# Optimization experiments

Hardware: AMD Instinct MI355X
Metric: run time of the kernel (lower is better)

## Reference

```python
import jax, jax.numpy as jnp
import numpy as np

IN_C = 128
KEY_C = 128
VAL_C = 128
HEADS = 8
N_CLS = 4

def setup_inputs() -> dict:
    key = jax.random.key(0)
    ks = jax.random.split(key, 10)
    n, c, d, h, w = 2, IN_C, 16, 64, 64
    x = jax.random.normal(ks[0], (n, c, d, h, w), dtype=jnp.float32)
    CLS = jax.random.normal(ks[1], (n, KEY_C, N_CLS), dtype=jnp.float32)
    s = 0.02
    Wk = jax.random.normal(ks[2], (KEY_C, IN_C), dtype=jnp.float32) * s
    bk = jnp.zeros((KEY_C,), dtype=jnp.float32)
    Wq = jax.random.normal(ks[3], (KEY_C, IN_C), dtype=jnp.float32) * s
    bq = jnp.zeros((KEY_C,), dtype=jnp.float32)
    Wv = jax.random.normal(ks[4], (VAL_C, IN_C), dtype=jnp.float32) * s
    bv = jnp.zeros((VAL_C,), dtype=jnp.float32)
    Wr = jax.random.normal(ks[5], (IN_C, VAL_C), dtype=jnp.float32) * s
    br = jnp.zeros((IN_C,), dtype=jnp.float32)
    return {"x": x, "CLS": CLS, "Wk": Wk, "bk": bk, "Wq": Wq, "bq": bq,
            "Wv": Wv, "bv": bv, "Wr": Wr, "br": br}

def reference(x, CLS, Wk, bk, Wq, bq, Wv, bv, Wr, br):
    n, c, d, h, w = x.shape
    L = d * h * w
    xf = x.reshape(n, c, L)
    # 1x1 Conv3d == channel matmul
    keys = jnp.einsum('oc,ncl->nol', Wk, xf) + bk[None, :, None]
    queries = jnp.einsum('oc,ncl->nol', Wq, xf) + bq[None, :, None]
    values = jnp.einsum('oc,ncl->nol', Wv, xf) + bv[None, :, None]
    # prepend CLS tokens along the sequence axis
    keys = jnp.concatenate([CLS, keys], axis=-1)      # (n, kc, L+4)
    queries = jnp.concatenate([CLS, queries], axis=-1)
    values = jnp.concatenate([CLS, values], axis=-1)
    Lt = L + N_CLS
    hk = KEY_C // HEADS
    hv = VAL_C // HEADS
    # contiguous channel slices per head == reshape (n, HEADS, hk, Lt)
    k = jax.nn.softmax(keys.reshape(n, HEADS, hk, Lt), axis=3)    # softmax over sequence
    q = jax.nn.softmax(queries.reshape(n, HEADS, hk, Lt), axis=2) # softmax over head channels
    v = values.reshape(n, HEADS, hv, Lt)
    context = jnp.einsum('nhkl,nhvl->nhkv', k, v)                 # (n, H, hk, hv)
    att = jnp.einsum('nhkv,nhkl->nhvl', context, q)               # (n, H, hv, Lt)
    # original loop reassigns CLS each head; final value comes from last head
    CLS_out = att[:, -1, :, :N_CLS]                               # (n, hv, 4)
    agg = att[:, :, :, N_CLS:].reshape(n, HEADS * hv, L)          # concat over heads
    attention = (jnp.einsum('oc,ncl->nol', Wr, agg) + br[None, :, None]).reshape(n, c, d, h, w)
    context_last = context[:, -1]                                 # last head's context
    return (attention, context_last, CLS_out)
```

## Files before the change

kernel.cpp:

```cpp
#include <hip/hip_runtime.h>

typedef unsigned short u16;
typedef short bf16x8 __attribute__((ext_vector_type(8)));
typedef float floatx4 __attribute__((ext_vector_type(4)));

#define OUT_CTX 16777216
#define OUT_CLS (OUT_CTX + 512)

__device__ __forceinline__ u16 f2b(float f) {
  unsigned int u = __float_as_uint(f);
  u += 0x7fffu + ((u >> 16) & 1u);
  return (u16)(u >> 16);
}
__device__ __forceinline__ float b2f(u16 b) { return __uint_as_float(((unsigned int)b) << 16); }

__device__ __forceinline__ float pack_val(const float* W, int eo) {
  int mt = eo >> 11;
  int rem = eo & 2047;
  int ks = rem >> 9;
  int lane = (rem >> 3) & 63;
  int j = rem & 7;
  int row = mt * 16 + (lane & 15);
  int col = ks * 32 + (lane >> 4) * 8 + j;
  return W[row * 128 + col];
}

__global__ __launch_bounds__(256) void kP(
    const float* __restrict__ Wk, const float* __restrict__ Wq,
    const float* __restrict__ Wv, const float* __restrict__ CLS,
    float* __restrict__ S2, float* __restrict__ Cnum2,
    u16* __restrict__ wkv, u16* __restrict__ wqf) {
  const int t = threadIdx.x;
  if (blockIdx.x < 24) {
    #pragma unroll
    for (int i = 0; i < 8; ++i) {
      int e = blockIdx.x * 2048 + i * 256 + t;
      if (e < 32768) {
        wkv[e] = f2b(pack_val(e < 16384 ? Wk : Wv, e & 16383));
      } else {
        wqf[e - 32768] = f2b(pack_val(Wq, e - 32768));
      }
    }
  } else {
    int nn = t >> 7, r = t & 127;
    float s = 0.f;
    #pragma unroll
    for (int j = 0; j < 4; ++j) s += __expf(CLS[(nn * 128 + r) * 4 + j]);
    S2[t] = s;
    S2[256 + t] = 0.f;
    S2[512 + t] = 0.f;
    S2[768 + t] = 0.f;
    for (int i = 0; i < 16; ++i) {
      int o = t * 16 + i;
      int n2 = o >> 11;
      int rem = o & 2047;
      int h = rem >> 8;
      int kc = (rem >> 4) & 15;
      int vc = rem & 15;
      float a = 0.f;
      #pragma unroll
      for (int j = 0; j < 4; ++j)
        a += __expf(CLS[(n2 * 128 + h * 16 + kc) * 4 + j]) *
             CLS[(n2 * 128 + h * 16 + vc) * 4 + j];
      Cnum2[o] = a;
      Cnum2[4096 + o] = 0.f;
      Cnum2[8192 + o] = 0.f;
      Cnum2[12288 + o] = 0.f;
    }
  }
}

__global__ __launch_bounds__(256) void kA(
    const float* __restrict__ x, const float* __restrict__ bk,
    const float* __restrict__ bv, float* __restrict__ S2,
    float* __restrict__ Cnum2, const u16* __restrict__ wkv) {
  __shared__ __align__(16) u16 xT[2][64][136];
  __shared__ __align__(16) u16 ev[256][72];
  const int t = threadIdx.x;
  const int w = t >> 6, lane = t & 63;
  const int quad = lane >> 4, lm = lane & 15;
  const int n = blockIdx.x >> 9;
  const int l0base = (blockIdx.x & 511) << 7;
  const int slot = blockIdx.x & 3;
  const int sc = t >> 4;
  const int sl4 = t & 15;

  float4 pf[8];
  #pragma unroll
  for (int i = 0; i < 8; ++i) {
    int c = i * 16 + sc;
    pf[i] = *(const float4*)(x + (((size_t)(n * 128 + c)) << 16) + l0base + sl4 * 4);
  }

  bf16x8 wf[4][4];
  #pragma unroll
  for (int mt = 0; mt < 4; ++mt) {
    int rb = (mt < 2) ? (2 * w + mt) : (8 + 2 * w + (mt - 2));
    #pragma unroll
    for (int ks = 0; ks < 4; ++ks)
      wf[mt][ks] = *(const bf16x8*)(wkv + (((rb * 4 + ks) * 64 + lane) * 8));
  }
  float bias_[4][4];
  #pragma unroll
  for (int mt = 0; mt < 4; ++mt)
    #pragma unroll
    for (int j = 0; j < 4; ++j) {
      int r = w * 32 + (mt & 1) * 16 + quad * 4 + j;
      bias_[mt][j] = (mt < 2) ? bk[r] : bv[r];
    }

  floatx4 z4 = {0.f, 0.f, 0.f, 0.f};
  floatx4 cacc[2] = {z4, z4};
  float sacc[2][4] = {{0.f, 0.f, 0.f, 0.f}, {0.f, 0.f, 0.f, 0.f}};

  for (int tile = 0; tile < 2; ++tile) {
    u16 (*xb)[136] = xT[tile];
    #pragma unroll
    for (int i = 0; i < 8; ++i) {
      int cc = i * 16 + sc;
      int col = sl4 * 4;
      xb[col + 0][cc] = f2b(pf[i].x);
      xb[col + 1][cc] = f2b(pf[i].y);
      xb[col + 2][cc] = f2b(pf[i].z);
      xb[col + 3][cc] = f2b(pf[i].w);
    }
    __syncthreads();

    floatx4 acc[4][4];
    #pragma unroll
    for (int mt = 0; mt < 4; ++mt)
      #pragma unroll
      for (int nt = 0; nt < 4; ++nt) acc[mt][nt] = z4;

    #pragma unroll
    for (int nt = 0; nt < 4; ++nt)
      #pragma unroll
      for (int ks = 0; ks < 4; ++ks) {
        bf16x8 b = *(const bf16x8*)(&xb[nt * 16 + lm][ks * 32 + quad * 8]);
        #pragma unroll
        for (int mt = 0; mt < 4; ++mt)
          acc[mt][nt] = __builtin_amdgcn_mfma_f32_16x16x32_bf16(wf[mt][ks], b, acc[mt][nt], 0, 0, 0);
      }

    if (tile == 0) {
      #pragma unroll
      for (int i = 0; i < 8; ++i) {
        int c = i * 16 + sc;
        pf[i] = *(const float4*)(x + (((size_t)(n * 128 + c)) << 16) + l0base + 64 + sl4 * 4);
      }
    }

    #pragma unroll
    for (int mt = 0; mt < 4; ++mt)
      #pragma unroll
      for (int j = 0; j < 4; ++j) {
        int R = ((mt < 2) ? 0 : 128) + w * 32 + (mt & 1) * 16 + quad * 4 + j;
        #pragma unroll
        for (int nt = 0; nt < 4; ++nt) {
          float v = acc[mt][nt][j] + bias_[mt][j];
          if (mt < 2) {
            v = __expf(v);
            u16 b = f2b(v);
            ev[R][nt * 16 + lm] = b;
            sacc[mt][j] += b2f(b);
          } else {
            ev[R][nt * 16 + lm] = f2b(v);
          }
        }
      }

    #pragma unroll
    for (int hh = 0; hh < 2; ++hh) {
      int h = w * 2 + hh;
      #pragma unroll
      for (int ks = 0; ks < 2; ++ks) {
        bf16x8 aE = *(const bf16x8*)(&ev[h * 16 + lm][ks * 32 + quad * 8]);
        bf16x8 bV = *(const bf16x8*)(&ev[128 + h * 16 + lm][ks * 32 + quad * 8]);
        cacc[hh] = __builtin_amdgcn_mfma_f32_16x16x32_bf16(aE, bV, cacc[hh], 0, 0, 0);
      }
    }
  }

  float* Cn = Cnum2 + slot * 4096;
  #pragma unroll
  for (int hh = 0; hh < 2; ++hh) {
    int h = w * 2 + hh;
    #pragma unroll
    for (int j = 0; j < 4; ++j)
      atomicAdd(&Cn[((n * 8 + h) * 16 + quad * 4 + j) * 16 + lm], cacc[hh][j]);
  }
  #pragma unroll
  for (int mt = 0; mt < 2; ++mt)
    #pragma unroll
    for (int j = 0; j < 4; ++j) {
      float s = sacc[mt][j];
      s += __shfl_xor(s, 1);
      s += __shfl_xor(s, 2);
      s += __shfl_xor(s, 4);
      s += __shfl_xor(s, 8);
      if (lm == 0)
        atomicAdd(&S2[slot * 256 + n * 128 + w * 32 + mt * 16 + quad * 4 + j], s);
    }
}

__global__ __launch_bounds__(256) void kM(
    const float* __restrict__ Wr, const float* __restrict__ CLS,
    const float* __restrict__ S2, const float* __restrict__ Cnum2,
    u16* __restrict__ mfrag, float* __restrict__ out) {
  __shared__ float ctxn[4096];
  const int t = threadIdx.x;
  float sinv = 1.f / (S2[t] + S2[256 + t] + S2[512 + t] + S2[768 + t]);
  #pragma unroll
  for (int i = 0; i < 16; ++i) {
    int o = t * 16 + i;
    ctxn[o] = (Cnum2[o] + Cnum2[4096 + o] + Cnum2[8192 + o] + Cnum2[12288 + o]) * sinv;
  }
  __syncthreads();

  if (blockIdx.x == 0) {
    for (int e = t; e < 512; e += 256) {
      int nn = e >> 8, kc = (e >> 4) & 15, vc = e & 15;
      out[OUT_CTX + e] = ctxn[((nn * 8 + 7) * 16 + kc) * 16 + vc];
    }
    if (t < 128) {
      int nn = t >> 6, vc = (t >> 2) & 15, j = t & 3;
      float den = 0.f, num = 0.f;
      #pragma unroll
      for (int kc = 0; kc < 16; ++kc) {
        float e_ = __expf(CLS[(nn * 128 + 112 + kc) * 4 + j]);
        den += e_;
        num += e_ * ctxn[((nn * 8 + 7) * 16 + kc) * 16 + vc];
      }
      out[OUT_CLS + t] = num / den;
    }
  }

  #pragma unroll
  for (int i = 0; i < 8; ++i) {
    int e = blockIdx.x * 2048 + i * 256 + t;
    int nn = e >> 14;
    int rem = e & 16383;
    int rb = rem >> 11;
    int ks = (rem >> 9) & 3;
    int ln = (rem >> 3) & 63;
    int j = rem & 7;
    int o = rb * 16 + (ln & 15);
    int cc = ks * 32 + (ln >> 4) * 8 + j;
    int h = cc >> 4, k = cc & 15;
    float m = 0.f;
    #pragma unroll
    for (int v = 0; v < 16; ++v)
      m += Wr[o * 128 + h * 16 + v] * ctxn[((nn * 8 + h) * 16 + k) * 16 + v];
    mfrag[e] = f2b(m);
  }
}

__global__ __launch_bounds__(256) void kB(
    const float* __restrict__ x, const float* __restrict__ bq,
    const float* __restrict__ br, const u16* __restrict__ wqf,
    const u16* __restrict__ mfrag, float* __restrict__ out) {
  __shared__ __align__(16) u16 xT[64][136];
  __shared__ __align__(16) u16 qT[64][136];
  const int t = threadIdx.x;
  const int w = t >> 6, lane = t & 63;
  const int quad = lane >> 4, lm = lane & 15;
  const int n = blockIdx.x >> 9;
  const int l0base = (blockIdx.x & 511) << 7;
  const int sc = t >> 4;
  const int sl4 = t & 15;

  float4 pf[8];
  #pragma unroll
  for (int i = 0; i < 8; ++i) {
    int c = i * 16 + sc;
    pf[i] = *(const float4*)(x + (((size_t)(n * 128 + c)) << 16) + l0base + sl4 * 4);
  }

  bf16x8 wq[2][4], mA[2][4];
  #pragma unroll
  for (int mt = 0; mt < 2; ++mt)
    #pragma unroll
    for (int ks = 0; ks < 4; ++ks) {
      wq[mt][ks] = *(const bf16x8*)(wqf + ((((w * 2 + mt) * 4 + ks) * 64 + lane) * 8));
      mA[mt][ks] = *(const bf16x8*)(mfrag + ((((n * 8 + w * 2 + mt) * 4 + ks) * 64 + lane) * 8));
    }

  float bqv_[2][4], brv[2][4];
  #pragma unroll
  for (int mt = 0; mt < 2; ++mt)
    #pragma unroll
    for (int j = 0; j < 4; ++j) {
      bqv_[mt][j] = bq[(w * 2 + mt) * 16 + quad * 4 + j];
      brv[mt][j] = br[(w * 2 + mt) * 16 + quad * 4 + j];
    }

  floatx4 z4 = {0.f, 0.f, 0.f, 0.f};

  for (int tile = 0; tile < 2; ++tile) {
    int l0 = l0base + tile * 64;
    #pragma unroll
    for (int i = 0; i < 8; ++i) {
      int cc = i * 16 + sc;
      int col = sl4 * 4;
      xT[col + 0][cc] = f2b(pf[i].x);
      xT[col + 1][cc] = f2b(pf[i].y);
      xT[col + 2][cc] = f2b(pf[i].z);
      xT[col + 3][cc] = f2b(pf[i].w);
    }
    __syncthreads();

    floatx4 acc[2][4];
    #pragma unroll
    for (int mt = 0; mt < 2; ++mt)
      #pragma unroll
      for (int nt = 0; nt < 4; ++nt) acc[mt][nt] = z4;

    #pragma unroll
    for (int nt = 0; nt < 4; ++nt)
      #pragma unroll
      for (int ks = 0; ks < 4; ++ks) {
        bf16x8 b = *(const bf16x8*)(&xT[nt * 16 + lm][ks * 32 + quad * 8]);
        #pragma unroll
        for (int mt = 0; mt < 2; ++mt)
          acc[mt][nt] = __builtin_amdgcn_mfma_f32_16x16x32_bf16(wq[mt][ks], b, acc[mt][nt], 0, 0, 0);
      }

    #pragma unroll
    for (int mt = 0; mt < 2; ++mt) {
      int h = w * 2 + mt;
      #pragma unroll
      for (int nt = 0; nt < 4; ++nt) {
        float e[4];
        float ssum = 0.f;
        #pragma unroll
        for (int j = 0; j < 4; ++j) {
          e[j] = __expf(acc[mt][nt][j] + bqv_[mt][j]);
          ssum += e[j];
        }
        ssum += __shfl_xor(ssum, 16);
        ssum += __shfl_xor(ssum, 32);
        float inv = 1.f / ssum;
        #pragma unroll
        for (int j = 0; j < 4; ++j)
          qT[nt * 16 + lm][h * 16 + quad * 4 + j] = f2b(e[j] * inv);
      }
    }

    if (tile == 0) {
      #pragma unroll
      for (int i = 0; i < 8; ++i) {
        int c = i * 16 + sc;
        pf[i] = *(const float4*)(x + (((size_t)(n * 128 + c)) << 16) + l0base + 64 + sl4 * 4);
      }
    }
    __syncthreads();

    floatx4 acc2[2][4];
    #pragma unroll
    for (int mt = 0; mt < 2; ++mt)
      #pragma unroll
      for (int nt = 0; nt < 4; ++nt) acc2[mt][nt] = z4;

    #pragma unroll
    for (int nt = 0; nt < 4; ++nt)
      #pragma unroll
      for (int ks = 0; ks < 4; ++ks) {
        bf16x8 b = *(const bf16x8*)(&qT[nt * 16 + lm][ks * 32 + quad * 8]);
        #pragma unroll
        for (int mt = 0; mt < 2; ++mt)
          acc2[mt][nt] = __builtin_amdgcn_mfma_f32_16x16x32_bf16(mA[mt][ks], b, acc2[mt][nt], 0, 0, 0);
      }

    #pragma unroll
    for (int mt = 0; mt < 2; ++mt)
      #pragma unroll
      for (int j = 0; j < 4; ++j) {
        int R = (w * 2 + mt) * 16 + quad * 4 + j;
        #pragma unroll
        for (int nt = 0; nt < 4; ++nt)
          out[(((size_t)(n * 128 + R)) << 16) + l0 + nt * 16 + lm] = acc2[mt][nt][j] + brv[mt][j];
      }
  }
}

extern "C" void kernel_launch(void* const* d_in, const int* in_sizes, int n_in,
                              void* d_out, int out_size, void* d_ws, size_t ws_size,
                              hipStream_t stream) {
  const float* x   = (const float*)d_in[0];
  const float* CLS = (const float*)d_in[1];
  const float* Wk  = (const float*)d_in[2];
  const float* bk  = (const float*)d_in[3];
  const float* Wq  = (const float*)d_in[4];
  const float* bq  = (const float*)d_in[5];
  const float* Wv  = (const float*)d_in[6];
  const float* bv  = (const float*)d_in[7];
  const float* Wr  = (const float*)d_in[8];
  const float* br  = (const float*)d_in[9];
  float* out = (float*)d_out;
  char* ws = (char*)d_ws;
  float* S2    = (float*)(ws + 0);
  float* Cnum2 = (float*)(ws + 4096);
  u16* wkv     = (u16*)(ws + 69632);
  u16* wqf     = (u16*)(ws + 135168);
  u16* mfrag   = (u16*)(ws + 167936);

  kP<<<25, 256, 0, stream>>>(Wk, Wq, Wv, CLS, S2, Cnum2, wkv, wqf);
  kA<<<1024, 256, 0, stream>>>(x, bk, bv, S2, Cnum2, wkv);
  kM<<<16, 256, 0, stream>>>(Wr, CLS, S2, Cnum2, mfrag, out);
  kB<<<1024, 256, 0, stream>>>(x, bq, br, wqf, mfrag, out);
}
```

Before: 195.8 us.

## Drop prep and merge kernels, pack weights inline, recompute context per block

```diff
diff --git a/kernel.cpp b/kernel.cpp
--- a/kernel.cpp
+++ b/kernel.cpp
@@ -2,6 +2,7 @@
 
 typedef unsigned short u16;
 typedef short bf16x8 __attribute__((ext_vector_type(8)));
+typedef short short4v __attribute__((ext_vector_type(4)));
 typedef float floatx4 __attribute__((ext_vector_type(4)));
 
 #define OUT_CTX 16777216
@@ -14,115 +15,70 @@
 }
 __device__ __forceinline__ float b2f(u16 b) { return __uint_as_float(((unsigned int)b) << 16); }
 
-__device__ __forceinline__ float pack_val(const float* W, int eo) {
-  int mt = eo >> 11;
-  int rem = eo & 2047;
-  int ks = rem >> 9;
-  int lane = (rem >> 3) & 63;
-  int j = rem & 7;
-  int row = mt * 16 + (lane & 15);
-  int col = ks * 32 + (lane >> 4) * 8 + j;
-  return W[row * 128 + col];
-}
-
-__global__ __launch_bounds__(256) void kP(
-    const float* __restrict__ Wk, const float* __restrict__ Wq,
-    const float* __restrict__ Wv, const float* __restrict__ CLS,
-    float* __restrict__ S2, float* __restrict__ Cnum2,
-    u16* __restrict__ wkv, u16* __restrict__ wqf) {
-  const int t = threadIdx.x;
-  if (blockIdx.x < 24) {
-    #pragma unroll
-    for (int i = 0; i < 8; ++i) {
-      int e = blockIdx.x * 2048 + i * 256 + t;
-      if (e < 32768) {
-        wkv[e] = f2b(pack_val(e < 16384 ? Wk : Wv, e & 16383));
-      } else {
-        wqf[e - 32768] = f2b(pack_val(Wq, e - 32768));
-      }
-    }
-  } else {
-    int nn = t >> 7, r = t & 127;
-    float s = 0.f;
-    #pragma unroll
-    for (int j = 0; j < 4; ++j) s += __expf(CLS[(nn * 128 + r) * 4 + j]);
-    S2[t] = s;
-    S2[256 + t] = 0.f;
-    S2[512 + t] = 0.f;
-    S2[768 + t] = 0.f;
-    for (int i = 0; i < 16; ++i) {
-      int o = t * 16 + i;
-      int n2 = o >> 11;
-      int rem = o & 2047;
-      int h = rem >> 8;
-      int kc = (rem >> 4) & 15;
-      int vc = rem & 15;
-      float a = 0.f;
-      #pragma unroll
-      for (int j = 0; j < 4; ++j)
-        a += __expf(CLS[(n2 * 128 + h * 16 + kc) * 4 + j]) *
-             CLS[(n2 * 128 + h * 16 + vc) * 4 + j];
-      Cnum2[o] = a;
-      Cnum2[4096 + o] = 0.f;
-      Cnum2[8192 + o] = 0.f;
-      Cnum2[12288 + o] = 0.f;
-    }
-  }
+__device__ __forceinline__ bf16x8 pack8(const float* p) {
+  float4 a = *(const float4*)p;
+  float4 b = *(const float4*)(p + 4);
+  bf16x8 r;
+  r[0] = (short)f2b(a.x); r[1] = (short)f2b(a.y); r[2] = (short)f2b(a.z); r[3] = (short)f2b(a.w);
+  r[4] = (short)f2b(b.x); r[5] = (short)f2b(b.y); r[6] = (short)f2b(b.z); r[7] = (short)f2b(b.w);
+  return r;
+}
+
+__device__ __forceinline__ float dot4(float4 a, float4 b) {
+  return a.x * b.x + a.y * b.y + a.z * b.z + a.w * b.w;
 }
 
 __global__ __launch_bounds__(256) void kA(
-    const float* __restrict__ x, const float* __restrict__ bk,
+    const float* __restrict__ x, const float* __restrict__ Wk,
+    const float* __restrict__ bk, const float* __restrict__ Wv,
     const float* __restrict__ bv, float* __restrict__ S2,
-    float* __restrict__ Cnum2, const u16* __restrict__ wkv) {
-  __shared__ __align__(16) u16 xT[2][64][136];
+    float* __restrict__ Cnum2) {
+  __shared__ __align__(16) u16 xT[64][136];
   __shared__ __align__(16) u16 ev[256][72];
   const int t = threadIdx.x;
   const int w = t >> 6, lane = t & 63;
   const int quad = lane >> 4, lm = lane & 15;
-  const int n = blockIdx.x >> 9;
-  const int l0base = (blockIdx.x & 511) << 7;
-  const int slot = blockIdx.x & 3;
-  const int sc = t >> 4;
-  const int sl4 = t & 15;
+  const int bid = blockIdx.x;
+  const int n = bid >> 8;
+  const int l0base = (bid & 255) << 8;
+  const int slot = bid & 3;
+  const int sc = t >> 4, sl4 = t & 15;
 
   float4 pf[8];
   #pragma unroll
-  for (int i = 0; i < 8; ++i) {
-    int c = i * 16 + sc;
-    pf[i] = *(const float4*)(x + (((size_t)(n * 128 + c)) << 16) + l0base + sl4 * 4);
-  }
+  for (int i = 0; i < 8; ++i)
+    pf[i] = *(const float4*)(x + (((size_t)(n * 128 + sc * 8 + i)) << 16) + l0base + sl4 * 4);
 
   bf16x8 wf[4][4];
   #pragma unroll
-  for (int mt = 0; mt < 4; ++mt) {
-    int rb = (mt < 2) ? (2 * w + mt) : (8 + 2 * w + (mt - 2));
+  for (int nt = 0; nt < 4; ++nt) {
+    const float* W = (nt < 2) ? Wk : Wv;
+    int row = w * 32 + (nt & 1) * 16 + lm;
     #pragma unroll
     for (int ks = 0; ks < 4; ++ks)
-      wf[mt][ks] = *(const bf16x8*)(wkv + (((rb * 4 + ks) * 64 + lane) * 8));
-  }
-  float bias_[4][4];
-  #pragma unroll
-  for (int mt = 0; mt < 4; ++mt)
-    #pragma unroll
-    for (int j = 0; j < 4; ++j) {
-      int r = w * 32 + (mt & 1) * 16 + quad * 4 + j;
-      bias_[mt][j] = (mt < 2) ? bk[r] : bv[r];
-    }
+      wf[nt][ks] = pack8(W + row * 128 + ks * 32 + quad * 8);
+  }
+  float biasE[2] = { bk[w * 32 + lm], bk[w * 32 + 16 + lm] };
+  float biasV[2] = { bv[w * 32 + lm], bv[w * 32 + 16 + lm] };
 
   floatx4 z4 = {0.f, 0.f, 0.f, 0.f};
   floatx4 cacc[2] = {z4, z4};
-  float sacc[2][4] = {{0.f, 0.f, 0.f, 0.f}, {0.f, 0.f, 0.f, 0.f}};
-
-  for (int tile = 0; tile < 2; ++tile) {
-    u16 (*xb)[136] = xT[tile];
-    #pragma unroll
-    for (int i = 0; i < 8; ++i) {
-      int cc = i * 16 + sc;
-      int col = sl4 * 4;
-      xb[col + 0][cc] = f2b(pf[i].x);
-      xb[col + 1][cc] = f2b(pf[i].y);
-      xb[col + 2][cc] = f2b(pf[i].z);
-      xb[col + 3][cc] = f2b(pf[i].w);
+  float sacc[2] = {0.f, 0.f};
+
+  for (int tile = 0; tile < 4; ++tile) {
+    const float* pff = (const float*)pf;
+    #pragma unroll
+    for (int r = 0; r < 4; ++r) {
+      bf16x8 vx;
+      #pragma unroll
+      for (int i = 0; i < 8; ++i) vx[i] = (short)f2b(pff[i * 4 + r]);
+      *(bf16x8*)&xT[sl4 * 4 + r][sc * 8] = vx;
+    }
+    if (tile < 3) {
+      int l0n = l0base + (tile + 1) * 64;
+      #pragma unroll
+      for (int i = 0; i < 8; ++i)
+        pf[i] = *(const float4*)(x + (((size_t)(n * 128 + sc * 8 + i)) << 16) + l0n + sl4 * 4);
     }
     __syncthreads();
 
@@ -133,40 +89,39 @@
       for (int nt = 0; nt < 4; ++nt) acc[mt][nt] = z4;
 
     #pragma unroll
-    for (int nt = 0; nt < 4; ++nt)
+    for (int mt = 0; mt < 4; ++mt)
       #pragma unroll
       for (int ks = 0; ks < 4; ++ks) {
-        bf16x8 b = *(const bf16x8*)(&xb[nt * 16 + lm][ks * 32 + quad * 8]);
-        #pragma unroll
-        for (int mt = 0; mt < 4; ++mt)
-          acc[mt][nt] = __builtin_amdgcn_mfma_f32_16x16x32_bf16(wf[mt][ks], b, acc[mt][nt], 0, 0, 0);
-      }
-
-    if (tile == 0) {
-      #pragma unroll
-      for (int i = 0; i < 8; ++i) {
-        int c = i * 16 + sc;
-        pf[i] = *(const float4*)(x + (((size_t)(n * 128 + c)) << 16) + l0base + 64 + sl4 * 4);
-      }
-    }
-
-    #pragma unroll
-    for (int mt = 0; mt < 4; ++mt)
-      #pragma unroll
-      for (int j = 0; j < 4; ++j) {
-        int R = ((mt < 2) ? 0 : 128) + w * 32 + (mt & 1) * 16 + quad * 4 + j;
-        #pragma unroll
-        for (int nt = 0; nt < 4; ++nt) {
-          float v = acc[mt][nt][j] + bias_[mt][j];
-          if (mt < 2) {
-            v = __expf(v);
-            u16 b = f2b(v);
-            ev[R][nt * 16 + lm] = b;
-            sacc[mt][j] += b2f(b);
-          } else {
-            ev[R][nt * 16 + lm] = f2b(v);
-          }
+        bf16x8 xa = *(const bf16x8*)&xT[mt * 16 + lm][ks * 32 + quad * 8];
+        #pragma unroll
+        for (int nt = 0; nt < 4; ++nt)
+          acc[mt][nt] = __builtin_amdgcn_mfma_f32_16x16x32_bf16(xa, wf[nt][ks], acc[mt][nt], 0, 0, 0);
+      }
+    __syncthreads();
+
+    #pragma unroll
+    for (int nt = 0; nt < 2; ++nt)
+      #pragma unroll
+      for (int mt = 0; mt < 4; ++mt) {
+        short4v p;
+        #pragma unroll
+        for (int j = 0; j < 4; ++j) {
+          float v = __expf(acc[mt][nt][j] + biasE[nt]);
+          u16 b = f2b(v);
+          sacc[nt] += b2f(b);
+          p[j] = (short)b;
         }
+        *(short4v*)&ev[w * 32 + nt * 16 + lm][mt * 16 + quad * 4] = p;
+      }
+    #pragma unroll
+    for (int nt = 0; nt < 2; ++nt)
+      #pragma unroll
+      for (int mt = 0; mt < 4; ++mt) {
+        short4v p;
+        #pragma unroll
+        for (int j = 0; j < 4; ++j)
+          p[j] = (short)f2b(acc[mt][nt + 2][j] + biasV[nt]);
+        *(short4v*)&ev[128 + w * 32 + nt * 16 + lm][mt * 16 + quad * 4] = p;
       }
 
     #pragma unroll
@@ -174,8 +129,8 @@
       int h = w * 2 + hh;
       #pragma unroll
       for (int ks = 0; ks < 2; ++ks) {
-        bf16x8 aE = *(const bf16x8*)(&ev[h * 16 + lm][ks * 32 + quad * 8]);
-        bf16x8 bV = *(const bf16x8*)(&ev[128 + h * 16 + lm][ks * 32 + quad * 8]);
+        bf16x8 aE = *(const bf16x8*)&ev[h * 16 + lm][ks * 32 + quad * 8];
+        bf16x8 bV = *(const bf16x8*)&ev[128 + h * 16 + lm][ks * 32 + quad * 8];
         cacc[hh] = __builtin_amdgcn_mfma_f32_16x16x32_bf16(aE, bV, cacc[hh], 0, 0, 0);
       }
     }
@@ -190,122 +145,143 @@
       atomicAdd(&Cn[((n * 8 + h) * 16 + quad * 4 + j) * 16 + lm], cacc[hh][j]);
   }
   #pragma unroll
-  for (int mt = 0; mt < 2; ++mt)
-    #pragma unroll
-    for (int j = 0; j < 4; ++j) {
-      float s = sacc[mt][j];
-      s += __shfl_xor(s, 1);
-      s += __shfl_xor(s, 2);
-      s += __shfl_xor(s, 4);
-      s += __shfl_xor(s, 8);
-      if (lm == 0)
-        atomicAdd(&S2[slot * 256 + n * 128 + w * 32 + mt * 16 + quad * 4 + j], s);
-    }
-}
-
-__global__ __launch_bounds__(256) void kM(
-    const float* __restrict__ Wr, const float* __restrict__ CLS,
+  for (int nt = 0; nt < 2; ++nt) {
+    float s = sacc[nt];
+    s += __shfl_xor(s, 16);
+    s += __shfl_xor(s, 32);
+    if (quad == 0)
+      atomicAdd(&S2[slot * 256 + n * 128 + w * 32 + nt * 16 + lm], s);
+  }
+}
+
+__global__ __launch_bounds__(256, 4) void kB(
+    const float* __restrict__ x, const float* __restrict__ CLS,
+    const float* __restrict__ Wq, const float* __restrict__ bq,
+    const float* __restrict__ Wr, const float* __restrict__ br,
     const float* __restrict__ S2, const float* __restrict__ Cnum2,
-    u16* __restrict__ mfrag, float* __restrict__ out) {
-  __shared__ float ctxn[4096];
-  const int t = threadIdx.x;
-  float sinv = 1.f / (S2[t] + S2[256 + t] + S2[512 + t] + S2[768 + t]);
-  #pragma unroll
-  for (int i = 0; i < 16; ++i) {
-    int o = t * 16 + i;
-    ctxn[o] = (Cnum2[o] + Cnum2[4096 + o] + Cnum2[8192 + o] + Cnum2[12288 + o]) * sinv;
-  }
-  __syncthreads();
-
-  if (blockIdx.x == 0) {
-    for (int e = t; e < 512; e += 256) {
-      int nn = e >> 8, kc = (e >> 4) & 15, vc = e & 15;
-      out[OUT_CTX + e] = ctxn[((nn * 8 + 7) * 16 + kc) * 16 + vc];
-    }
-    if (t < 128) {
-      int nn = t >> 6, vc = (t >> 2) & 15, j = t & 3;
-      float den = 0.f, num = 0.f;
-      #pragma unroll
-      for (int kc = 0; kc < 16; ++kc) {
-        float e_ = __expf(CLS[(nn * 128 + 112 + kc) * 4 + j]);
-        den += e_;
-        num += e_ * ctxn[((nn * 8 + 7) * 16 + kc) * 16 + vc];
-      }
-      out[OUT_CLS + t] = num / den;
-    }
-  }
-
-  #pragma unroll
-  for (int i = 0; i < 8; ++i) {
-    int e = blockIdx.x * 2048 + i * 256 + t;
-    int nn = e >> 14;
-    int rem = e & 16383;
-    int rb = rem >> 11;
-    int ks = (rem >> 9) & 3;
-    int ln = (rem >> 3) & 63;
-    int j = rem & 7;
-    int o = rb * 16 + (ln & 15);
-    int cc = ks * 32 + (ln >> 4) * 8 + j;
-    int h = cc >> 4, k = cc & 15;
-    float m = 0.f;
-    #pragma unroll
-    for (int v = 0; v < 16; ++v)
-      m += Wr[o * 128 + h * 16 + v] * ctxn[((nn * 8 + h) * 16 + k) * 16 + v];
-    mfrag[e] = f2b(m);
-  }
-}
-
-__global__ __launch_bounds__(256) void kB(
-    const float* __restrict__ x, const float* __restrict__ bq,
-    const float* __restrict__ br, const u16* __restrict__ wqf,
-    const u16* __restrict__ mfrag, float* __restrict__ out) {
+    float* __restrict__ out) {
   __shared__ __align__(16) u16 xT[64][136];
-  __shared__ __align__(16) u16 qT[64][136];
+  __shared__ __align__(16) u16 ubuf[64 * 136];
   const int t = threadIdx.x;
   const int w = t >> 6, lane = t & 63;
   const int quad = lane >> 4, lm = lane & 15;
-  const int n = blockIdx.x >> 9;
-  const int l0base = (blockIdx.x & 511) << 7;
-  const int sc = t >> 4;
-  const int sl4 = t & 15;
+  const int bid = blockIdx.x;
+  const int n = bid >> 9;
+  const int l0base = (bid & 511) << 7;
+  const int sc = t >> 4, sl4 = t & 15;
 
   float4 pf[8];
   #pragma unroll
-  for (int i = 0; i < 8; ++i) {
-    int c = i * 16 + sc;
-    pf[i] = *(const float4*)(x + (((size_t)(n * 128 + c)) << 16) + l0base + sl4 * 4);
-  }
-
-  bf16x8 wq[2][4], mA[2][4];
+  for (int i = 0; i < 8; ++i)
+    pf[i] = *(const float4*)(x + (((size_t)(n * 128 + sc * 8 + i)) << 16) + l0base + sl4 * 4);
+
+  bf16x8 wq[2][4];
+  #pragma unroll
+  for (int mt = 0; mt < 2; ++mt) {
+    int row = (w * 2 + mt) * 16 + lm;
+    #pragma unroll
+    for (int ks = 0; ks < 4; ++ks)
+      wq[mt][ks] = pack8(Wq + row * 128 + ks * 32 + quad * 8);
+  }
+  float bqv[2][4], brv[2][4];
   #pragma unroll
   for (int mt = 0; mt < 2; ++mt)
     #pragma unroll
-    for (int ks = 0; ks < 4; ++ks) {
-      wq[mt][ks] = *(const bf16x8*)(wqf + ((((w * 2 + mt) * 4 + ks) * 64 + lane) * 8));
-      mA[mt][ks] = *(const bf16x8*)(mfrag + ((((n * 8 + w * 2 + mt) * 4 + ks) * 64 + lane) * 8));
-    }
-
-  float bqv_[2][4], brv[2][4];
-  #pragma unroll
-  for (int mt = 0; mt < 2; ++mt)
-    #pragma unroll
     for (int j = 0; j < 4; ++j) {
-      bqv_[mt][j] = bq[(w * 2 + mt) * 16 + quad * 4 + j];
+      bqv[mt][j] = bq[(w * 2 + mt) * 16 + quad * 4 + j];
       brv[mt][j] = br[(w * 2 + mt) * 16 + quad * 4 + j];
     }
 
+  float* ctxn = (float*)ubuf;
+  {
+    int hk = t >> 1, v0 = (t & 1) * 8;
+    int hbase = hk & 0x70;
+    float ek[4];
+    float den = 0.f;
+    #pragma unroll
+    for (int j = 0; j < 4; ++j) {
+      ek[j] = __expf(CLS[(n * 128 + hk) * 4 + j]);
+      den += ek[j];
+    }
+    #pragma unroll
+    for (int s = 0; s < 4; ++s) den += S2[s * 256 + n * 128 + hk];
+    float inv = 1.f / den;
+    float vv[8];
+    #pragma unroll
+    for (int i = 0; i < 8; ++i) {
+      int v = v0 + i;
+      float num = 0.f;
+      #pragma unroll
+      for (int s = 0; s < 4; ++s) num += Cnum2[s * 4096 + (n * 128 + hk) * 16 + v];
+      #pragma unroll
+      for (int j = 0; j < 4; ++j) num += ek[j] * CLS[(n * 128 + hbase + v) * 4 + j];
+      vv[i] = num * inv;
+    }
+    float4 a = {vv[0], vv[1], vv[2], vv[3]}, b = {vv[4], vv[5], vv[6], vv[7]};
+    *(float4*)&ctxn[hk * 16 + v0] = a;
+    *(float4*)&ctxn[hk * 16 + v0 + 4] = b;
+  }
+  __syncthreads();
+
+  if ((bid & 511) == 0) {
+    {
+      int kc = t >> 4, vc = t & 15;
+      out[OUT_CTX + n * 256 + t] = ctxn[(112 + kc) * 16 + vc];
+    }
+    if (t < 64) {
+      int vc = t >> 2, j = t & 3;
+      float den = 0.f, num = 0.f;
+      #pragma unroll
+      for (int kc = 0; kc < 16; ++kc) {
+        float e_ = __expf(CLS[(n * 128 + 112 + kc) * 4 + j]);
+        den += e_;
+        num += e_ * ctxn[(112 + kc) * 16 + vc];
+      }
+      out[OUT_CLS + n * 64 + t] = num / den;
+    }
+  }
+
+  bf16x8 mA[2][4];
+  for (int ks = 0; ks < 4; ++ks) {
+    int h = 2 * ks + (quad >> 1);
+    float4 wrv[2][4];
+    #pragma unroll
+    for (int mt = 0; mt < 2; ++mt) {
+      const float* wp = Wr + ((w * 2 + mt) * 16 + lm) * 128 + h * 16;
+      #pragma unroll
+      for (int q4 = 0; q4 < 4; ++q4) wrv[mt][q4] = *(const float4*)(wp + q4 * 4);
+    }
+    short mr0[8], mr1[8];
+    #pragma unroll
+    for (int jj = 0; jj < 8; ++jj) {
+      int k = (quad & 1) * 8 + jj;
+      const float4* cp = (const float4*)&ctxn[(h * 16 + k) * 16];
+      float4 c0 = cp[0], c1 = cp[1], c2 = cp[2], c3 = cp[3];
+      float m0 = dot4(wrv[0][0], c0) + dot4(wrv[0][1], c1) + dot4(wrv[0][2], c2) + dot4(wrv[0][3], c3);
+      float m1 = dot4(wrv[1][0], c0) + dot4(wrv[1][1], c1) + dot4(wrv[1][2], c2) + dot4(wrv[1][3], c3);
+      mr0[jj] = (short)f2b(m0);
+      mr1[jj] = (short)f2b(m1);
+    }
+    mA[0][ks] = *(bf16x8*)mr0;
+    mA[1][ks] = *(bf16x8*)mr1;
+  }
+
+  u16 (*qT)[136] = (u16 (*)[136])ubuf;
   floatx4 z4 = {0.f, 0.f, 0.f, 0.f};
-
   for (int tile = 0; tile < 2; ++tile) {
     int l0 = l0base + tile * 64;
-    #pragma unroll
-    for (int i = 0; i < 8; ++i) {
-      int cc = i * 16 + sc;
-      int col = sl4 * 4;
-      xT[col + 0][cc] = f2b(pf[i].x);
-      xT[col + 1][cc] = f2b(pf[i].y);
-      xT[col + 2][cc] = f2b(pf[i].z);
-      xT[col + 3][cc] = f2b(pf[i].w);
+    const float* pff = (const float*)pf;
+    #pragma unroll
+    for (int r = 0; r < 4; ++r) {
+      bf16x8 vx;
+      #pragma unroll
+      for (int i = 0; i < 8; ++i) vx[i] = (short)f2b(pff[i * 4 + r]);
+      *(bf16x8*)&xT[sl4 * 4 + r][sc * 8] = vx;
+    }
+    if (tile < 1) {
+      #pragma unroll
+      for (int i = 0; i < 8; ++i)
+        pf[i] = *(const float4*)(x + (((size_t)(n * 128 + sc * 8 + i)) << 16) + l0base + 64 + sl4 * 4);
     }
     __syncthreads();
 
@@ -319,7 +295,7 @@
     for (int nt = 0; nt < 4; ++nt)
       #pragma unroll
       for (int ks = 0; ks < 4; ++ks) {
-        bf16x8 b = *(const bf16x8*)(&xT[nt * 16 + lm][ks * 32 + quad * 8]);
+        bf16x8 b = *(const bf16x8*)&xT[nt * 16 + lm][ks * 32 + quad * 8];
         #pragma unroll
         for (int mt = 0; mt < 2; ++mt)
           acc[mt][nt] = __builtin_amdgcn_mfma_f32_16x16x32_bf16(wq[mt][ks], b, acc[mt][nt], 0, 0, 0);
@@ -334,23 +310,16 @@
         float ssum = 0.f;
         #pragma unroll
         for (int j = 0; j < 4; ++j) {
-          e[j] = __expf(acc[mt][nt][j] + bqv_[mt][j]);
+          e[j] = __expf(acc[mt][nt][j] + bqv[mt][j]);
           ssum += e[j];
         }
         ssum += __shfl_xor(ssum, 16);
         ssum += __shfl_xor(ssum, 32);
         float inv = 1.f / ssum;
-        #pragma unroll
-        for (int j = 0; j < 4; ++j)
-          qT[nt * 16 + lm][h * 16 + quad * 4 + j] = f2b(e[j] * inv);
-      }
-    }
-
-    if (tile == 0) {
-      #pragma unroll
-      for (int i = 0; i < 8; ++i) {
-        int c = i * 16 + sc;
-        pf[i] = *(const float4*)(x + (((size_t)(n * 128 + c)) << 16) + l0base + 64 + sl4 * 4);
+        short4v p;
+        #pragma unroll
+        for (int j = 0; j < 4; ++j) p[j] = (short)f2b(e[j] * inv);
+        *(short4v*)&qT[nt * 16 + lm][h * 16 + quad * 4] = p;
       }
     }
     __syncthreads();
@@ -365,7 +334,7 @@
     for (int nt = 0; nt < 4; ++nt)
       #pragma unroll
       for (int ks = 0; ks < 4; ++ks) {
-        bf16x8 b = *(const bf16x8*)(&qT[nt * 16 + lm][ks * 32 + quad * 8]);
+        bf16x8 b = *(const bf16x8*)&qT[nt * 16 + lm][ks * 32 + quad * 8];
         #pragma unroll
         for (int mt = 0; mt < 2; ++mt)
           acc2[mt][nt] = __builtin_amdgcn_mfma_f32_16x16x32_bf16(mA[mt][ks], b, acc2[mt][nt], 0, 0, 0);
@@ -400,12 +369,8 @@
   char* ws = (char*)d_ws;
   float* S2    = (float*)(ws + 0);
   float* Cnum2 = (float*)(ws + 4096);
-  u16* wkv     = (u16*)(ws + 69632);
-  u16* wqf     = (u16*)(ws + 135168);
-  u16* mfrag   = (u16*)(ws + 167936);
-
-  kP<<<25, 256, 0, stream>>>(Wk, Wq, Wv, CLS, S2, Cnum2, wkv, wqf);
-  kA<<<1024, 256, 0, stream>>>(x, bk, bv, S2, Cnum2, wkv);
-  kM<<<16, 256, 0, stream>>>(Wr, CLS, S2, Cnum2, mfrag, out);
-  kB<<<1024, 256, 0, stream>>>(x, bq, br, wqf, mfrag, out);
-}
+
+  hipMemsetAsync(ws, 0, 69632, stream);
+  kA<<<512, 256, 0, stream>>>(x, Wk, bk, Wv, bv, S2, Cnum2);
+  kB<<<1024, 256, 0, stream>>>(x, CLS, Wq, bq, Wr, br, S2, Cnum2, out);
+}
```

Measured after the change: 383.5 us. 95.9% more time.
